# Kernel optimization log

Measured on AMD Instinct MI355X. Metric: run time of the kernel, lower is better.

## Reference

```python
import jax, jax.numpy as jnp
import numpy as np

C, D, K15, K16, OUT = 64, 8, 15, 16, 512
B = 32768


def setup_inputs() -> dict:
    key = jax.random.key(0)
    kx, kS, kH, kT, kL = jax.random.split(key, 5)
    x = jax.random.normal(kx, (B, C * D), dtype=jnp.float32)
    S = jax.random.normal(kS, (C, D, K15), dtype=jnp.float32)
    H = jax.random.normal(kH, (K15, K16), dtype=jnp.float32)
    T = jax.random.normal(kT, (C, K15), dtype=jnp.float32)
    LUT = jax.random.normal(kL, (C, K16, OUT), dtype=jnp.float32)
    return {"x": x, "S": S, "H": H, "T": T, "LUT": LUT}


def reference(x, S, H, T, LUT):
    b = x.shape[0]
    xv = x.reshape(b, C, D)                              # (B, C, D)
    p = jnp.einsum('bcd,cdk->bck', xv, S) - T            # (B, C, 15)
    # torch sets zeros to -1 before sign => sign(x)==-1 when x<=0
    s = jnp.where(p > 0, jnp.float32(1.0), jnp.float32(-1.0))
    h = jnp.einsum('bck,kj->bcj', s, H)                  # (B, C, 16)
    idx = jnp.argmax(h, axis=-1)                         # (B, C) int
    # one_hot @ LUT == direct gather of LUT[c, idx[b,c], :]
    vals = LUT[jnp.arange(C)[None, :], idx]              # (B, C, OUT)
    return jnp.sum(vals, axis=1)                         # (B, OUT)
```

## Files before the change

kernel.cpp:

```cpp
#include <hip/hip_runtime.h>
#include <stdint.h>

#define B_    32768
#define C_    64
#define D_    8
#define K15_  15
#define K16_  16
#define OUT_  512

typedef _Float16 half4v __attribute__((ext_vector_type(4)));
typedef _Float16 half8  __attribute__((ext_vector_type(8)));

#define AMAP_OFF  0
#define AMAP_SZ   32768
#define S64_OFF   32768
#define S64_SZ    (64 * 15 * 8 * 8)
#define T64_OFF   (S64_OFF + S64_SZ)
#define T64_SZ    (64 * 15 * 8)
#define IDX_OFF   (T64_OFF + T64_SZ)
#define IDX_SZ    (B_ * C_)
#define PCT_OFF   (IDX_OFF + IDX_SZ)
#define PCT_SZ    (B_ * 32)
#define PTAB_OFF  (PCT_OFF + PCT_SZ)
#define PTAB_SZ   (32 * 32 * 256 * 16 * 2)
#define WS_NEED   ((size_t)PTAB_OFF + PTAB_SZ)

__global__ __launch_bounds__(256) void k_setup(const float* __restrict__ LUT,
                                               const float* __restrict__ H,
                                               const float* __restrict__ S,
                                               const float* __restrict__ T,
                                               _Float16* __restrict__ P5,
                                               uint8_t* __restrict__ amap,
                                               double* __restrict__ S64,
                                               double* __restrict__ T64,
                                               int do_pairs) {
    int gid = blockIdx.x * 256 + threadIdx.x;

    if (do_pairs) {
        int e8 = gid & 1;
        int q = (gid >> 1) & 255;
        int jc = (gid >> 9) & 31;
        int p = gid >> 14;
        int t0 = q >> 4;
        int t1 = q & 15;
        int j0 = jc * 16 + e8 * 8;
        const float* u = LUT + (size_t)((2 * p) * 16 + t0) * 512 + j0;
        const float* v = LUT + (size_t)((2 * p + 1) * 16 + t1) * 512 + j0;
        float4 u0 = ((const float4*)u)[0];
        float4 u1 = ((const float4*)u)[1];
        float4 v0 = ((const float4*)v)[0];
        float4 v1 = ((const float4*)v)[1];
        half8 w;
        w[0] = (_Float16)(u0.x + v0.x);
        w[1] = (_Float16)(u0.y + v0.y);
        w[2] = (_Float16)(u0.z + v0.z);
        w[3] = (_Float16)(u0.w + v0.w);
        w[4] = (_Float16)(u1.x + v1.x);
        w[5] = (_Float16)(u1.y + v1.y);
        w[6] = (_Float16)(u1.z + v1.z);
        w[7] = (_Float16)(u1.w + v1.w);
        *(half8*)(P5 + (size_t)gid * 8) = w;
    }

    if (blockIdx.x < 128) {
        int code = gid;
        double h[K16_];
#pragma unroll
        for (int j = 0; j < K16_; ++j) h[j] = 0.0;
#pragma unroll
        for (int k = 0; k < K15_; ++k) {
            double s = ((code >> k) & 1) ? 1.0 : -1.0;
#pragma unroll
            for (int j = 0; j < K16_; ++j) h[j] += s * (double)H[k * K16_ + j];
        }
        double best = h[0];
        int bi = 0;
#pragma unroll
        for (int j = 1; j < K16_; ++j) {
            if (h[j] > best) { best = h[j]; bi = j; }
        }
        amap[code] = (uint8_t)bi;
    } else if (blockIdx.x == 128) {
        for (int i = threadIdx.x; i < 64 * 15 * 8; i += 256) {
            int c = i / 120;
            int r = i - c * 120;
            int k = r >> 3;
            int d = r & 7;
            S64[i] = (double)S[c * 120 + d * 15 + k];
        }
        for (int i = threadIdx.x; i < 64 * 15; i += 256) T64[i] = (double)T[i];
    }
}

#define XSTRIDE 585
__global__ __launch_bounds__(256) void k_codes2(const float* __restrict__ x,
                                                const double* __restrict__ S64,
                                                const double* __restrict__ T64,
                                                const uint8_t* __restrict__ amap,
                                                uint8_t* __restrict__ idxo,
                                                uint8_t* __restrict__ pcT) {
    __shared__ float xls[32 * XSTRIDE];
    __shared__ uint8_t idsh[64 * 68];

    int b0 = blockIdx.x * 64;
    int lane = threadIdx.x & 63;
    int wv = __builtin_amdgcn_readfirstlane(threadIdx.x >> 6);

    for (int half = 0; half < 2; ++half) {
        __syncthreads();
#pragma unroll
        for (int t = 0; t < 16; ++t) {
            int e = t * 256 + threadIdx.x;
            int b = e >> 6;
            int j4 = e & 63;
            float4 v = ((const float4*)(x + (size_t)(b0 + b) * 512 +
                                        half * 256))[j4];
            int cl = j4 >> 1;
            int d0 = (j4 & 1) * 4;
            float* dst = &xls[cl * XSTRIDE + b * 9 + d0];
            dst[0] = v.x; dst[1] = v.y; dst[2] = v.z; dst[3] = v.w;
        }
        __syncthreads();
        for (int i = 0; i < 8; ++i) {
            int cl = wv + i * 4;
            int c = half * 32 + cl;
            const double* Sc = S64 + c * 120;
            const double* Tc = T64 + c * 15;
            double xd[8];
#pragma unroll
            for (int d = 0; d < 8; ++d)
                xd[d] = (double)xls[cl * XSTRIDE + lane * 9 + d];
            unsigned code = 0;
#pragma unroll
            for (int k = 0; k < K15_; ++k) {
                double p = -Tc[k];
#pragma unroll
                for (int d = 0; d < 8; ++d) p = fma(xd[d], Sc[k * 8 + d], p);
                code |= (p > 0.0) ? (1u << k) : 0u;
            }
            idsh[lane * 68 + c] = amap[code];
        }
    }
    __syncthreads();

    int bb = threadIdx.x >> 2;
    int q = threadIdx.x & 3;
    {
        uint32_t w0 = *(const uint32_t*)&idsh[bb * 68 + q * 16 + 0];
        uint32_t w1 = *(const uint32_t*)&idsh[bb * 68 + q * 16 + 4];
        uint32_t w2 = *(const uint32_t*)&idsh[bb * 68 + q * 16 + 8];
        uint32_t w3 = *(const uint32_t*)&idsh[bb * 68 + q * 16 + 12];
        uint32_t* o = (uint32_t*)(idxo + (size_t)(b0 + bb) * 64 + q * 16);
        o[0] = w0; o[1] = w1; o[2] = w2; o[3] = w3;
    }
    {
        int row = b0 + bb;
        int rg = row >> 10;
        int tr = row & 127;
        int i_ = (row & 1023) >> 7;
        uint8_t* base = pcT + rg * 1024 + tr * 8 + i_;
#pragma unroll
        for (int pi = 0; pi < 8; ++pi) {
            int p = q * 8 + pi;
            uint8_t byte = (uint8_t)((idsh[bb * 68 + 2 * p] << 4) |
                                     idsh[bb * 68 + 2 * p + 1]);
            base[p * 32768] = byte;
        }
    }
}

__global__ __launch_bounds__(256, 4) void k_main6(const uint8_t* __restrict__ pcT,
                                                  const _Float16* __restrict__ P5,
                                                  float* __restrict__ out) {
    __shared__ alignas(16) _Float16 slab[2][256 * 24];

    int rg = blockIdx.x >> 5;
    int jc = blockIdx.x & 31;
    int t = threadIdx.x;
    int tc = t & 1;
    int tr = t >> 1;

    const _Float16* src0 = P5 + ((size_t)(0 * 32 + jc) * 256 + t) * 16;
    const uint8_t* cbase = pcT + rg * 1024 + tr * 8;

    float acc[8][8];
#pragma unroll
    for (int i = 0; i < 8; ++i)
#pragma unroll
        for (int e = 0; e < 8; ++e) acc[i][e] = 0.f;

    half8 g0 = ((const half8*)src0)[0];
    half8 g1 = ((const half8*)src0)[1];
    uint64_t cw = *(const uint64_t*)cbase;

    for (int p = 0; p < 32; ++p) {
        _Float16* wb = &slab[p & 1][0];
        *(half8*)(wb + t * 24) = g0;
        *(half8*)(wb + t * 24 + 8) = g1;

        uint64_t cw_cur = cw;
        if (p < 31) {
            const _Float16* srcn =
                P5 + ((size_t)((p + 1) * 32 + jc) * 256 + t) * 16;
            g0 = ((const half8*)srcn)[0];
            g1 = ((const half8*)srcn)[1];
            cw = *(const uint64_t*)(cbase + (size_t)(p + 1) * 32768);
        }

        __syncthreads();

        const _Float16* rb = &slab[p & 1][0] + tc * 8;
#pragma unroll
        for (int i = 0; i < 8; ++i) {
            int ci = (int)((cw_cur >> (8 * i)) & 0xFF);
            half8 v = *(const half8*)(rb + ci * 24);
#pragma unroll
            for (int e = 0; e < 8; ++e) acc[i][e] += (float)v[e];
        }
    }

#pragma unroll
    for (int i = 0; i < 8; ++i) {
        int row = rg * 1024 + i * 128 + tr;
        float* o = out + (size_t)row * 512 + jc * 16 + tc * 8;
        float4 w0;
        w0.x = acc[i][0]; w0.y = acc[i][1]; w0.z = acc[i][2]; w0.w = acc[i][3];
        float4 w1;
        w1.x = acc[i][4]; w1.y = acc[i][5]; w1.z = acc[i][6]; w1.w = acc[i][7];
        ((float4*)o)[0] = w0;
        ((float4*)o)[1] = w1;
    }
}

__global__ __launch_bounds__(256) void k_main_direct(const uint8_t* __restrict__ idx,
                                                     const float* __restrict__ LUT,
                                                     float* __restrict__ out) {
    int j4 = threadIdx.x & 127;
    int sub = threadIdx.x >> 7;
    int b0 = blockIdx.x * 16 + sub * 8;
    const float4* L4 = (const float4*)LUT;
    for (int r = 0; r < 8; ++r) {
        int b = b0 + r;
        const uint32_t* iw = (const uint32_t*)(idx + (size_t)b * 64);
        float4 acc;
        acc.x = 0.f; acc.y = 0.f; acc.z = 0.f; acc.w = 0.f;
#pragma unroll
        for (int i = 0; i < 16; ++i) {
            uint32_t w = __builtin_amdgcn_readfirstlane(iw[i]);
#pragma unroll
            for (int t = 0; t < 4; ++t) {
                int c = i * 4 + t;
                uint32_t codev = (w >> (8 * t)) & 0xFu;
                float4 v = L4[(size_t)(c * 16 + codev) * 128 + j4];
                acc.x += v.x; acc.y += v.y; acc.z += v.z; acc.w += v.w;
            }
        }
        ((float4*)(out + (size_t)b * 512))[j4] = acc;
    }
}

extern "C" void kernel_launch(void* const* d_in, const int* in_sizes, int n_in,
                              void* d_out, int out_size, void* d_ws, size_t ws_size,
                              hipStream_t stream) {
    const float* x   = (const float*)d_in[0];
    const float* S   = (const float*)d_in[1];
    const float* H   = (const float*)d_in[2];
    const float* T   = (const float*)d_in[3];
    const float* LUT = (const float*)d_in[4];
    float* out = (float*)d_out;

    uint8_t* ws = (uint8_t*)d_ws;
    uint8_t* amap = ws + AMAP_OFF;
    double* S64   = (double*)(ws + S64_OFF);
    double* T64   = (double*)(ws + T64_OFF);
    uint8_t* idxb = ws + IDX_OFF;
    uint8_t* pcTb = ws + PCT_OFF;
    _Float16* P5  = (_Float16*)(ws + PTAB_OFF);

    bool use_pairs = ws_size >= WS_NEED;

    hipLaunchKernelGGL(k_setup, dim3(use_pairs ? 2048 : 129), dim3(256), 0,
                       stream, LUT, H, S, T, P5, amap, S64, T64,
                       use_pairs ? 1 : 0);
    hipLaunchKernelGGL(k_codes2, dim3(B_ / 64), dim3(256), 0, stream,
                       x, S64, T64, amap, idxb, pcTb);
    if (use_pairs) {
        hipLaunchKernelGGL(k_main6, dim3(1024), dim3(256), 0, stream,
                           pcTb, P5, out);
    } else {
        hipLaunchKernelGGL(k_main_direct, dim3(B_ / 16), dim3(256), 0, stream,
                           idxb, LUT, out);
    }
}
```

Before: 189.2 us.

## Use fp32 projections with fp64 fallback, skip idx write, split main kernel rows

The code computation now runs the 15 projections in fp32 and falls back to fp64 only when some projection lies near zero (below 1e-4). This is meant to cut the cost of fp64 FMAs on the hot path. When the pairs path is used it also skips writing the byte index buffer, and it reuses that space for the fp32 S and T copies. The main gather kernel is split so each block handles 4 row groups instead of 8, with twice as many blocks and a higher occupancy hint. The fp32 fast path risks sign mismatches if fp32 error exceeds the fallback threshold.

Result: no change. 189.8 us (+0.3%).

```diff
diff --git a/kernel.cpp b/kernel.cpp
--- a/kernel.cpp
+++ b/kernel.cpp
@@ -19,6 +19,7 @@
 #define T64_SZ    (64 * 15 * 8)
 #define IDX_OFF   (T64_OFF + T64_SZ)
 #define IDX_SZ    (B_ * C_)
+#define S32_SZ    (64 * 15 * 8 * 4)
 #define PCT_OFF   (IDX_OFF + IDX_SZ)
 #define PCT_SZ    (B_ * 32)
 #define PTAB_OFF  (PCT_OFF + PCT_SZ)
@@ -33,6 +34,8 @@
                                                uint8_t* __restrict__ amap,
                                                double* __restrict__ S64,
                                                double* __restrict__ T64,
+                                               float* __restrict__ S32,
+                                               float* __restrict__ T32,
                                                int do_pairs) {
     int gid = blockIdx.x * 256 + threadIdx.x;
 
@@ -86,16 +89,24 @@
             int r = i - c * 120;
             int k = r >> 3;
             int d = r & 7;
-            S64[i] = (double)S[c * 120 + d * 15 + k];
-        }
-        for (int i = threadIdx.x; i < 64 * 15; i += 256) T64[i] = (double)T[i];
+            float sv = S[c * 120 + d * 15 + k];
+            S64[i] = (double)sv;
+            if (do_pairs) S32[i] = sv;
+        }
+        for (int i = threadIdx.x; i < 64 * 15; i += 256) {
+            T64[i] = (double)T[i];
+            if (do_pairs) T32[i] = T[i];
+        }
     }
 }
 
 #define XSTRIDE 585
+template <int FAST>
 __global__ __launch_bounds__(256) void k_codes2(const float* __restrict__ x,
                                                 const double* __restrict__ S64,
                                                 const double* __restrict__ T64,
+                                                const float* __restrict__ S32,
+                                                const float* __restrict__ T32,
                                                 const uint8_t* __restrict__ amap,
                                                 uint8_t* __restrict__ idxo,
                                                 uint8_t* __restrict__ pcT) {
@@ -124,19 +135,52 @@
         for (int i = 0; i < 8; ++i) {
             int cl = wv + i * 4;
             int c = half * 32 + cl;
-            const double* Sc = S64 + c * 120;
-            const double* Tc = T64 + c * 15;
-            double xd[8];
-#pragma unroll
-            for (int d = 0; d < 8; ++d)
-                xd[d] = (double)xls[cl * XSTRIDE + lane * 9 + d];
             unsigned code = 0;
-#pragma unroll
-            for (int k = 0; k < K15_; ++k) {
-                double p = -Tc[k];
-#pragma unroll
-                for (int d = 0; d < 8; ++d) p = fma(xd[d], Sc[k * 8 + d], p);
-                code |= (p > 0.0) ? (1u << k) : 0u;
+            if (FAST) {
+                const float* Sc = S32 + c * 120;
+                const float* Tc = T32 + c * 15;
+                float xf[8];
+#pragma unroll
+                for (int d = 0; d < 8; ++d)
+                    xf[d] = xls[cl * XSTRIDE + lane * 9 + d];
+                float pmin = 3.0e38f;
+#pragma unroll
+                for (int k = 0; k < K15_; ++k) {
+                    float p = -Tc[k];
+#pragma unroll
+                    for (int d = 0; d < 8; ++d)
+                        p = fmaf(xf[d], Sc[k * 8 + d], p);
+                    code |= (p > 0.f) ? (1u << k) : 0u;
+                    pmin = fminf(pmin, fabsf(p));
+                }
+                if (pmin < 1e-4f) {
+                    const double* Sd = S64 + c * 120;
+                    const double* Td = T64 + c * 15;
+                    code = 0;
+#pragma unroll
+                    for (int k = 0; k < K15_; ++k) {
+                        double p = -Td[k];
+#pragma unroll
+                        for (int d = 0; d < 8; ++d)
+                            p = fma((double)xf[d], Sd[k * 8 + d], p);
+                        code |= (p > 0.0) ? (1u << k) : 0u;
+                    }
+                }
+            } else {
+                const double* Sc = S64 + c * 120;
+                const double* Tc = T64 + c * 15;
+                double xd[8];
+#pragma unroll
+                for (int d = 0; d < 8; ++d)
+                    xd[d] = (double)xls[cl * XSTRIDE + lane * 9 + d];
+#pragma unroll
+                for (int k = 0; k < K15_; ++k) {
+                    double p = -Tc[k];
+#pragma unroll
+                    for (int d = 0; d < 8; ++d)
+                        p = fma(xd[d], Sc[k * 8 + d], p);
+                    code |= (p > 0.0) ? (1u << k) : 0u;
+                }
             }
             idsh[lane * 68 + c] = amap[code];
         }
@@ -145,7 +189,7 @@
 
     int bb = threadIdx.x >> 2;
     int q = threadIdx.x & 3;
-    {
+    if (!FAST) {
         uint32_t w0 = *(const uint32_t*)&idsh[bb * 68 + q * 16 + 0];
         uint32_t w1 = *(const uint32_t*)&idsh[bb * 68 + q * 16 + 4];
         uint32_t w2 = *(const uint32_t*)&idsh[bb * 68 + q * 16 + 8];
@@ -169,59 +213,60 @@
     }
 }
 
-__global__ __launch_bounds__(256, 4) void k_main6(const uint8_t* __restrict__ pcT,
+__global__ __launch_bounds__(256, 6) void k_main7(const uint8_t* __restrict__ pcT,
                                                   const _Float16* __restrict__ P5,
                                                   float* __restrict__ out) {
     __shared__ alignas(16) _Float16 slab[2][256 * 24];
 
-    int rg = blockIdx.x >> 5;
+    int rg5 = blockIdx.x >> 5;
     int jc = blockIdx.x & 31;
     int t = threadIdx.x;
     int tc = t & 1;
     int tr = t >> 1;
 
-    const _Float16* src0 = P5 + ((size_t)(0 * 32 + jc) * 256 + t) * 16;
-    const uint8_t* cbase = pcT + rg * 1024 + tr * 8;
-
-    float acc[8][8];
-#pragma unroll
-    for (int i = 0; i < 8; ++i)
+    const uint8_t* cbase = pcT + (rg5 >> 1) * 1024 + tr * 8 + (rg5 & 1) * 4;
+
+    float acc[4][8];
+#pragma unroll
+    for (int i = 0; i < 4; ++i)
 #pragma unroll
         for (int e = 0; e < 8; ++e) acc[i][e] = 0.f;
 
+    const _Float16* src0 = P5 + ((size_t)jc * 256 + t) * 16;
     half8 g0 = ((const half8*)src0)[0];
     half8 g1 = ((const half8*)src0)[1];
-    uint64_t cw = *(const uint64_t*)cbase;
+    uint32_t cw = *(const uint32_t*)cbase;
 
     for (int p = 0; p < 32; ++p) {
         _Float16* wb = &slab[p & 1][0];
         *(half8*)(wb + t * 24) = g0;
         *(half8*)(wb + t * 24 + 8) = g1;
 
-        uint64_t cw_cur = cw;
+        uint32_t cw_cur = cw;
         if (p < 31) {
             const _Float16* srcn =
                 P5 + ((size_t)((p + 1) * 32 + jc) * 256 + t) * 16;
             g0 = ((const half8*)srcn)[0];
             g1 = ((const half8*)srcn)[1];
-            cw = *(const uint64_t*)(cbase + (size_t)(p + 1) * 32768);
+            cw = *(const uint32_t*)(cbase + (size_t)(p + 1) * 32768);
         }
 
         __syncthreads();
 
         const _Float16* rb = &slab[p & 1][0] + tc * 8;
 #pragma unroll
-        for (int i = 0; i < 8; ++i) {
+        for (int i = 0; i < 4; ++i) {
             int ci = (int)((cw_cur >> (8 * i)) & 0xFF);
             half8 v = *(const half8*)(rb + ci * 24);
 #pragma unroll
-            for (int e = 0; e < 8; ++e) acc[i][e] += (float)v[e];
-        }
-    }
-
-#pragma unroll
-    for (int i = 0; i < 8; ++i) {
-        int row = rg * 1024 + i * 128 + tr;
+            for (int e = 0; e < 8; ++e)
+                acc[i][e] = fmaf((float)v[e], 1.0f, acc[i][e]);
+        }
+    }
+
+#pragma unroll
+    for (int i = 0; i < 4; ++i) {
+        int row = rg5 * 512 + i * 128 + tr;
         float* o = out + (size_t)row * 512 + jc * 16 + tc * 8;
         float4 w0;
         w0.x = acc[i][0]; w0.y = acc[i][1]; w0.z = acc[i][2]; w0.w = acc[i][3];
@@ -274,20 +319,24 @@
     double* S64   = (double*)(ws + S64_OFF);
     double* T64   = (double*)(ws + T64_OFF);
     uint8_t* idxb = ws + IDX_OFF;
+    float* S32    = (float*)(ws + IDX_OFF);
+    float* T32    = (float*)(ws + IDX_OFF + S32_SZ);
     uint8_t* pcTb = ws + PCT_OFF;
     _Float16* P5  = (_Float16*)(ws + PTAB_OFF);
 
     bool use_pairs = ws_size >= WS_NEED;
 
     hipLaunchKernelGGL(k_setup, dim3(use_pairs ? 2048 : 129), dim3(256), 0,
-                       stream, LUT, H, S, T, P5, amap, S64, T64,
+                       stream, LUT, H, S, T, P5, amap, S64, T64, S32, T32,
                        use_pairs ? 1 : 0);
-    hipLaunchKernelGGL(k_codes2, dim3(B_ / 64), dim3(256), 0, stream,
-                       x, S64, T64, amap, idxb, pcTb);
     if (use_pairs) {
-        hipLaunchKernelGGL(k_main6, dim3(1024), dim3(256), 0, stream,
+        hipLaunchKernelGGL((k_codes2<1>), dim3(B_ / 64), dim3(256), 0, stream,
+                           x, S64, T64, S32, T32, amap, idxb, pcTb);
+        hipLaunchKernelGGL(k_main7, dim3(2048), dim3(256), 0, stream,
                            pcTb, P5, out);
     } else {
+        hipLaunchKernelGGL((k_codes2<0>), dim3(B_ / 64), dim3(256), 0, stream,
+                           x, S64, T64, S32, T32, amap, idxb, pcTb);
         hipLaunchKernelGGL(k_main_direct, dim3(B_ / 16), dim3(256), 0, stream,
                            idxb, LUT, out);
     }
```
